# Kernel optimization log

Measured on AMD Instinct MI355X. Metric: run time of the kernel, lower is better.

The kernel has to match this reference:

```python
import jax, jax.numpy as jnp
import numpy as np

N, E = 50000, 500000
A, R, EB, EH, H, C, AH, SH, S, AV = 64, 20, 32, 64, 4, 32, 128, 64, 32, 32
EPS = 1e-8
MAX_DIST = 0.5   # nm, maximum_interaction_radius
SCALE = 1.0      # nm, scale_factor


def physnet_rbf(d):
    # PhysNet radial basis: exp(-beta * (exp(-d) - mu_k)^2), mu_k in [exp(-r_cut), 1]
    mu = jnp.linspace(np.exp(-MAX_DIST), 1.0, R).astype(jnp.float32)
    beta = jnp.float32((2.0 / R * (1.0 - np.exp(-MAX_DIST))) ** -2)
    return jnp.exp(-beta * (jnp.exp(-d)[:, None] - mu) ** 2)  # [E, R]


def _forward(h, x, v, idx_i, idx_j, W_edge_in, b_edge_in, W_edge_h, b_edge_h,
             W_edge_out, b_edge_out, W_att, b_att, W_x_mix, W_node1, b_node1,
             W_node2, b_node2, W_post1, b_post1, W_post2, b_post2,
             W_vel1, b_vel1, W_vel2, w_v_mix):
    n = h.shape[0]
    act = jax.nn.silu
    seg_sum = lambda t, idx: jax.ops.segment_sum(t, idx, num_segments=n)

    # geometry
    r_ij = x[idx_j] - x[idx_i]                       # [E,3]
    d_ij = jnp.sqrt(jnp.sum(r_ij * r_ij, -1) + EPS)  # [E]
    dir_ij = r_ij / (d_ij[:, None] + EPS)            # [E,3]

    # update_edge: gather, RBF filter, edge MLP
    h_cat = jnp.concatenate([h[idx_i], h[idx_j]], -1)                 # [E,2A]
    filtered = physnet_rbf(d_ij) * (h_cat @ W_edge_in + b_edge_in)    # [E,R]
    e_in = jnp.concatenate([h_cat, filtered, d_ij[:, None] / SCALE], -1)
    h_ij_edge = act(e_in @ W_edge_h + b_edge_h) @ W_edge_out + b_edge_out  # [E,EB]

    # semantic attention: CELU logits + segment softmax over receivers per head
    logits = jax.nn.celu(h_ij_edge @ W_att + b_att, alpha=2.0)        # [E,H]
    seg_max = jax.ops.segment_max(logits, idx_i, num_segments=n)      # [n,H]
    exp_l = jnp.exp(logits - seg_max[idx_i])
    denom = seg_sum(exp_l, idx_i)
    att = exp_l / (denom[idx_i] + EPS)                                # [E,H]
    h_ij_semantic = (att[:, :, None] * h_ij_edge[:, None, :]).reshape(-1, H * EB)

    # neighborhood aggregation (scatter-add)
    h_i_semantic = seg_sum(h_ij_semantic, idx_i)                      # [n,H*EB]

    # spatial attention
    mix = jnp.tanh(h_ij_semantic @ W_x_mix)                           # [E,C]
    combinations = dir_ij[:, None, :] * mix[:, :, None]               # [E,C,3]
    counts = jnp.maximum(seg_sum(jnp.ones((idx_i.shape[0],), h.dtype), idx_i), 1.0)
    comb_mean = seg_sum(combinations, idx_i) / counts[:, None, None]  # scatter-mean
    comb_norm2 = jnp.sum(comb_mean * comb_mean, -1)                   # [n,C]
    h_i_spatial = act(act(comb_norm2 @ W_post1 + b_post1) @ W_post2 + b_post2)

    # node update (residual)
    node_in = jnp.concatenate([h, h_i_semantic, h_i_spatial], -1)
    h_upd = h + act(act(node_in @ W_node1 + b_node1) @ W_node2 + b_node2)

    # velocity / coordinate update
    v_ij = jnp.einsum('ecx,c->ex', combinations, w_v_mix)             # [E,3]
    dv = seg_sum(v_ij, idx_i) / counts[:, None]                       # scatter-mean
    gate = 2.0 * jax.nn.sigmoid(act(h_upd @ W_vel1 + b_vel1) @ W_vel2)  # [n,1]
    v_upd = gate * v + dv
    x_upd = x + v_upd
    return h_upd, x_upd, v_upd


def _p(k, shape, scale=0.05):
    return jax.random.normal(k, shape, dtype=jnp.float32) * scale


def setup_inputs() -> dict:
    key = jax.random.key(0)
    ks = jax.random.split(key, 24)
    return {
        'h': jax.random.normal(ks[0], (N, A), dtype=jnp.float32),
        'x': jax.random.normal(ks[1], (N, 3), dtype=jnp.float32),
        'v': jax.random.normal(ks[2], (N, 3), dtype=jnp.float32),
        'idx_i': jax.random.randint(ks[3], (E,), 0, N),
        'idx_j': jax.random.randint(ks[4], (E,), 0, N),
        'W_edge_in': _p(ks[5], (2 * A, R)), 'b_edge_in': jnp.zeros((R,), jnp.float32),
        'W_edge_h': _p(ks[6], (2 * A + R + 1, EH)), 'b_edge_h': jnp.zeros((EH,), jnp.float32),
        'W_edge_out': _p(ks[7], (EH, EB)), 'b_edge_out': jnp.zeros((EB,), jnp.float32),
        'W_att': _p(ks[8], (EB, H)), 'b_att': jnp.zeros((H,), jnp.float32),
        'W_x_mix': _p(ks[9], (H * EB, C)),
        'W_node1': _p(ks[10], (A + H * EB + S, AH)), 'b_node1': jnp.zeros((AH,), jnp.float32),
        'W_node2': _p(ks[11], (AH, A)), 'b_node2': jnp.zeros((A,), jnp.float32),
        'W_post1': _p(ks[12], (C, SH)), 'b_post1': jnp.zeros((SH,), jnp.float32),
        'W_post2': _p(ks[13], (SH, S)), 'b_post2': jnp.zeros((S,), jnp.float32),
        'W_vel1': _p(ks[14], (A, AV)), 'b_vel1': jnp.zeros((AV,), jnp.float32),
        'W_vel2': _p(ks[15], (AV, 1)),
        'w_v_mix': _p(ks[16], (C,)),
    }


def reference(h, x, v, idx_i, idx_j, W_edge_in, b_edge_in, W_edge_h, b_edge_h,
              W_edge_out, b_edge_out, W_att, b_att, W_x_mix, W_node1, b_node1,
              W_node2, b_node2, W_post1, b_post1, W_post2, b_post2,
              W_vel1, b_vel1, W_vel2, w_v_mix):
    return _forward(h, x, v, idx_i, idx_j, W_edge_in, b_edge_in, W_edge_h, b_edge_h,
                    W_edge_out, b_edge_out, W_att, b_att, W_x_mix, W_node1, b_node1,
                    W_node2, b_node2, W_post1, b_post1, W_post2, b_post2,
                    W_vel1, b_vel1, W_vel2, w_v_mix)
```

## Files before the change

### kernel.cpp

```cpp
#include <hip/hip_runtime.h>
#include <math.h>

#define DA 64
#define NODEIN_DIM 224
#define EPSC 1e-8f

typedef short v8s __attribute__((ext_vector_type(8)));
typedef float v4f __attribute__((ext_vector_type(4)));
typedef unsigned short ushort_t;

__device__ __forceinline__ float siluf(float v) {
  return v * __builtin_amdgcn_rcpf(1.0f + __expf(-v));
}
__device__ __forceinline__ float tanhfast(float x) {
  return 1.0f - 2.0f * __builtin_amdgcn_rcpf(__expf(2.0f * x) + 1.0f);
}

__device__ __forceinline__ void atomAddF(float* p, float v) {
#if defined(__HIP_DEVICE_COMPILE__)
  unsafeAtomicAdd(p, v);
#else
  atomicAdd(p, v);
#endif
}

__device__ __forceinline__ unsigned short f2bfu(float f) {
  union { float f; unsigned u; } v; v.f = f;
  unsigned r = v.u + 0x7fffu + ((v.u >> 16) & 1u);
  return (unsigned short)(r >> 16);
}
__device__ __forceinline__ short f2bfs(float f) { return (short)f2bfu(f); }
__device__ __forceinline__ float bf2f(ushort_t s) {
  union { unsigned u; float f; } v; v.u = ((unsigned)s) << 16; return v.f;
}

#define MU0 0.60653065971263342f
#define DMU ((1.0f - 0.60653065971263342f) / 19.0f)
#define BETA ((float)(1.0 / (0.039346934028736658 * 0.039346934028736658)))

__global__ __launch_bounds__(256) void cast_count(
    const float* __restrict__ hsrc, ushort_t* __restrict__ hb, int n4,
    const int* __restrict__ idx_i, int* __restrict__ deg, int E)
{
  const int stride = gridDim.x * blockDim.x;
  for (int i = blockIdx.x * blockDim.x + threadIdx.x; i < n4; i += stride) {
    const float4 fv = ((const float4*)hsrc)[i];
    ushort4 o;
    o.x = f2bfu(fv.x); o.y = f2bfu(fv.y); o.z = f2bfu(fv.z); o.w = f2bfu(fv.w);
    ((ushort4*)hb)[i] = o;
  }
  for (int e = blockIdx.x * blockDim.x + threadIdx.x; e < E; e += stride)
    atomicAdd(&deg[idx_i[e]], 1);
}

#define SCAN_B 64
#define SCAN_T (SCAN_B * 256)

__global__ __launch_bounds__(256) void deg_tsum(
    const int* __restrict__ deg, int* __restrict__ tsum, int N, int C)
{
  const int g = blockIdx.x * blockDim.x + threadIdx.x;
  const int lo = g * C;
  const int hi = (lo + C < N) ? (lo + C) : N;
  int s = 0;
  for (int i = lo; i < hi; ++i) s += deg[i];
  tsum[g] = s;
}

__global__ __launch_bounds__(256) void scan_tsum(int* __restrict__ tsum)
{
  __shared__ int ps[256];
  const int t = threadIdx.x;
  const int per = SCAN_T / 256;
  const int lo = t * per;
  int s = 0;
  for (int i = 0; i < per; ++i) s += tsum[lo + i];
  ps[t] = s;
  __syncthreads();
  if (t == 0) {
    int a = 0;
    for (int i = 0; i < 256; ++i) { const int v = ps[i]; ps[i] = a; a += v; }
  }
  __syncthreads();
  int acc = ps[t];
  for (int i = 0; i < per; ++i) {
    const int v = tsum[lo + i];
    tsum[lo + i] = acc;
    acc += v;
  }
}

__global__ __launch_bounds__(256) void write_csr(
    const int* __restrict__ deg, const int* __restrict__ tpre,
    int* __restrict__ rowstart, int* __restrict__ cursor, int N, int C)
{
  const int g = blockIdx.x * blockDim.x + threadIdx.x;
  const int lo = g * C;
  const int hi = (lo + C < N) ? (lo + C) : N;
  int acc = tpre[g];
  for (int i = lo; i < hi; ++i) {
    const int d = deg[i];
    rowstart[i] = acc;
    cursor[i] = acc;
    acc += d;
  }
  if (hi == N) rowstart[N] = acc;
}

__global__ __launch_bounds__(256) void bucket_edges(
    const int* __restrict__ idx_i, const int* __restrict__ idx_j,
    int* __restrict__ cursor, int* __restrict__ iperm,
    int* __restrict__ jperm, int E)
{
  const int stride = gridDim.x * blockDim.x;
  for (int e = blockIdx.x * blockDim.x + threadIdx.x; e < E; e += stride) {
    const int ii = idx_i[e];
    const int pos = atomicAdd(&cursor[ii], 1);
    iperm[pos] = ii;
    jperm[pos] = idx_j[e];
  }
}

#define THS 72
__global__ __launch_bounds__(512, 6) void edge_f12(
    const ushort_t* __restrict__ h_bf, const float* __restrict__ x,
    const int* __restrict__ iperm, const int* __restrict__ jperm,
    const float* __restrict__ W_in, const float* __restrict__ b_in,
    const float* __restrict__ W_h, const float* __restrict__ b_h,
    const float* __restrict__ W_out, const float* __restrict__ b_out,
    const float* __restrict__ W_att, const float* __restrict__ b_att,
    float* __restrict__ dirb, ushort_t* __restrict__ heb,
    float* __restrict__ expl, float* __restrict__ denom, int E)
{
  __shared__ ushort_t sB1[8 * 512];
  __shared__ ushort_t sB2[20 * 512];
  __shared__ ushort_t tH[8][16 * THS];

  const int tid = threadIdx.x;
  const int bsz = blockDim.x;
  for (int idx = tid; idx < 8 * 512; idx += bsz) {
    const int j = idx & 7;
    const int ln = (idx >> 3) & 63;
    const int f = idx >> 9;
    const int k = (f >> 1) * 32 + (ln >> 4) * 8 + j;
    const int col = (f & 1) * 16 + (ln & 15);
    sB1[idx] = (col < 20) ? f2bfu(W_in[k * 20 + col]) : (ushort_t)0;
  }
  for (int idx = tid; idx < 20 * 512; idx += bsz) {
    const int j = idx & 7;
    const int ln = (idx >> 3) & 63;
    const int f = idx >> 9;
    const int k = (f >> 2) * 32 + (ln >> 4) * 8 + j;
    const int col = (f & 3) * 16 + (ln & 15);
    sB2[idx] = (k < 149) ? f2bfu(W_h[k * 64 + col]) : (ushort_t)0;
  }
  __syncthreads();

  const int gtid = blockIdx.x * blockDim.x + tid;
  const int wid = gtid >> 6;
  const int lane = tid & 63;
  const int w = tid >> 6;
  const int nw = (gridDim.x * blockDim.x) >> 6;
  const int l15 = lane & 15;
  const int q = lane >> 4;

  const ushort_t* b1l = sB1 + lane * 8;
  const ushort_t* b2l = sB2 + lane * 8;

  v8s bfr3[2][2];
  #pragma unroll
  for (int kc = 0; kc < 2; ++kc)
    #pragma unroll
    for (int nt = 0; nt < 2; ++nt)
      #pragma unroll
      for (int j = 0; j < 8; ++j) {
        const int k = kc * 32 + q * 8 + j;
        const int col = nt * 16 + l15;
        bfr3[kc][nt][j] = f2bfs(W_out[k * 32 + col]);
      }

  float bin[2], mu[2];
  #pragma unroll
  for (int nt = 0; nt < 2; ++nt) {
    const int col = nt * 16 + l15;
    bin[nt] = (col < 20) ? b_in[col] : 0.0f;
    mu[nt] = MU0 + (float)col * DMU;
  }
  float bias2[4];
  #pragma unroll
  for (int nt = 0; nt < 4; ++nt) bias2[nt] = b_h[nt * 16 + l15];
  float bias3[2];
  #pragma unroll
  for (int nt = 0; nt < 2; ++nt) bias3[nt] = b_out[nt * 16 + l15];

  v8s battf;
  #pragma unroll
  for (int j = 0; j < 8; ++j)
    battf[j] = (l15 < 4) ? f2bfs(W_att[(q * 8 + j) * 4 + l15]) : (short)0;
  const float bav = (l15 < 4) ? b_att[l15] : 0.0f;

  const int ntiles = (E + 15) >> 4;

  int iiC = 0, jjC = 0;
  v8s afr[4];
  float rCx = 0.f, rCy = 0.f, rCz = 0.f;
  if (wid < ntiles) {
    const int row0 = wid * 16 + l15;
    const int rowL0 = (row0 < E) ? row0 : (E - 1);
    iiC = iperm[rowL0];
    jjC = jperm[rowL0];
    afr[0] = *(const v8s*)(h_bf + (size_t)iiC * 64 + q * 8);
    afr[1] = *(const v8s*)(h_bf + (size_t)iiC * 64 + 32 + q * 8);
    afr[2] = *(const v8s*)(h_bf + (size_t)jjC * 64 + q * 8);
    afr[3] = *(const v8s*)(h_bf + (size_t)jjC * 64 + 32 + q * 8);
    if (lane < 16) {
      rCx = x[jjC * 3 + 0] - x[iiC * 3 + 0];
      rCy = x[jjC * 3 + 1] - x[iiC * 3 + 1];
      rCz = x[jjC * 3 + 2] - x[iiC * 3 + 2];
    }
  }

  for (int t = wid; t < ntiles; t += nw) {
    const int tn = t + nw;
    int iiN = 0, jjN = 0;
    v8s nfr[4];
    float rNx = 0.f, rNy = 0.f, rNz = 0.f;
    if (tn < ntiles) {
      const int rowN = tn * 16 + l15;
      const int rowLN = (rowN < E) ? rowN : (E - 1);
      iiN = iperm[rowLN];
      jjN = jperm[rowLN];
      nfr[0] = *(const v8s*)(h_bf + (size_t)iiN * 64 + q * 8);
      nfr[1] = *(const v8s*)(h_bf + (size_t)iiN * 64 + 32 + q * 8);
      nfr[2] = *(const v8s*)(h_bf + (size_t)jjN * 64 + q * 8);
      nfr[3] = *(const v8s*)(h_bf + (size_t)jjN * 64 + 32 + q * 8);
      if (lane < 16) {
        rNx = x[jjN * 3 + 0] - x[iiN * 3 + 0];
        rNy = x[jjN * 3 + 1] - x[iiN * 3 + 1];
        rNz = x[jjN * 3 + 2] - x[iiN * 3 + 2];
      }
    }

    const int row = t * 16 + l15;
    float dval = 0.0f;
    if (lane < 16) {
      const float s2 = rCx * rCx + rCy * rCy + rCz * rCz + EPSC;
      const float rv = __builtin_amdgcn_rsqf(s2);
      dval = s2 * rv;
      if (row < E) {
        dirb[row * 3 + 0] = rCx * rv;
        dirb[row * 3 + 1] = rCy * rv;
        dirb[row * 3 + 2] = rCz * rv;
      }
    }

    v4f acc1[2];
    #pragma unroll
    for (int nt = 0; nt < 2; ++nt) {
      v4f a = {0.f, 0.f, 0.f, 0.f};
      #pragma unroll
      for (int kc = 0; kc < 4; ++kc) {
        const v8s bfrag = *(const v8s*)(b1l + (kc * 2 + nt) * 512);
        a = __builtin_amdgcn_mfma_f32_16x16x32_bf16(afr[kc], bfrag, a, 0, 0, 0);
      }
      acc1[nt] = a;
    }

    float dr[4], edr[4];
    #pragma unroll
    for (int r = 0; r < 4; ++r) {
      dr[r] = __shfl(dval, q * 4 + r);
      edr[r] = __expf(-dr[r]);
    }
    #pragma unroll
    for (int nt = 0; nt < 2; ++nt) {
      const int col = nt * 16 + l15;
      #pragma unroll
      for (int r = 0; r < 4; ++r) {
        ushort_t ov;
        if (col < 20) {
          const float tt = edr[r] - mu[nt];
          ov = f2bfu((acc1[nt][r] + bin[nt]) * __expf(-BETA * tt * tt));
        } else if (col == 20) {
          ov = f2bfu(dr[r]);
        } else {
          ov = 0;
        }
        tH[w][(q * 4 + r) * THS + col] = ov;
      }
    }
    __builtin_amdgcn_wave_barrier();

    const v8s afr4 = *(const v8s*)&tH[w][l15 * THS + q * 8];
    __builtin_amdgcn_wave_barrier();

    v4f acc2[4];
    #pragma unroll
    for (int nt = 0; nt < 4; ++nt) {
      v4f a = {0.f, 0.f, 0.f, 0.f};
      #pragma unroll
      for (int kc = 0; kc < 4; ++kc) {
        const v8s bfrag = *(const v8s*)(b2l + (kc * 4 + nt) * 512);
        a = __builtin_amdgcn_mfma_f32_16x16x32_bf16(afr[kc], bfrag, a, 0, 0, 0);
      }
      const v8s bfrag4 = *(const v8s*)(b2l + (4 * 4 + nt) * 512);
      a = __builtin_amdgcn_mfma_f32_16x16x32_bf16(afr4, bfrag4, a, 0, 0, 0);
      acc2[nt] = a;
    }

    #pragma unroll
    for (int nt = 0; nt < 4; ++nt) {
      #pragma unroll
      for (int r = 0; r < 4; ++r)
        tH[w][(q * 4 + r) * THS + nt * 16 + l15] =
            f2bfu(siluf(acc2[nt][r] + bias2[nt]));
    }
    __builtin_amdgcn_wave_barrier();

    v8s af3[2];
    af3[0] = *(const v8s*)&tH[w][l15 * THS + q * 8];
    af3[1] = *(const v8s*)&tH[w][l15 * THS + 32 + q * 8];

    v4f acc3[2];
    #pragma unroll
    for (int nt = 0; nt < 2; ++nt) {
      v4f a = {0.f, 0.f, 0.f, 0.f};
      #pragma unroll
      for (int kc = 0; kc < 2; ++kc)
        a = __builtin_amdgcn_mfma_f32_16x16x32_bf16(af3[kc], bfr3[kc][nt], a, 0, 0, 0);
      acc3[nt] = a;
    }
    __builtin_amdgcn_wave_barrier();

    const int rowb = t * 16 + q * 4;
    #pragma unroll
    for (int nt = 0; nt < 2; ++nt) {
      const int col = nt * 16 + l15;
      #pragma unroll
      for (int r = 0; r < 4; ++r) {
        const ushort_t hv = f2bfu(acc3[nt][r] + bias3[nt]);
        tH[w][(q * 4 + r) * THS + col] = hv;
        if (rowb + r < E) heb[(size_t)(rowb + r) * 32 + col] = hv;
      }
    }
    __builtin_amdgcn_wave_barrier();

    const v8s afA = *(const v8s*)&tH[w][l15 * THS + q * 8];
    v4f az = {0.f, 0.f, 0.f, 0.f};
    const v4f aacc = __builtin_amdgcn_mfma_f32_16x16x32_bf16(afA, battf, az, 0, 0, 0);

    int ii_r[4];
    #pragma unroll
    for (int r = 0; r < 4; ++r) ii_r[r] = __shfl(iiC, q * 4 + r);

    if (l15 < 4) {
      #pragma unroll
      for (int r = 0; r < 4; ++r) {
        if (rowb + r < E) {
          const float la = aacc[r] + bav;
          const float l = (la > 0.f) ? la : 2.0f * (__expf(0.5f * la) - 1.0f);
          const float ev = __expf(l);
          expl[(size_t)(rowb + r) * 4 + l15] = ev;
          atomAddF(&denom[ii_r[r] * 4 + l15], ev);
        }
      }
    }
    __builtin_amdgcn_wave_barrier();

    iiC = iiN; jjC = jjN;
    afr[0] = nfr[0]; afr[1] = nfr[1]; afr[2] = nfr[2]; afr[3] = nfr[3];
    rCx = rNx; rCy = rNy; rCz = rNz;
  }
}

__global__ __launch_bounds__(256) void node_fused(
    const int* __restrict__ rowstart,
    const ushort_t* __restrict__ heb,
    const float* __restrict__ expl, const float* __restrict__ denom,
    const float* __restrict__ dirb,
    const float* __restrict__ W_xmix, const float* __restrict__ w_vmix,
    ushort_t* __restrict__ hsem, float* __restrict__ norm2,
    float* __restrict__ dv_mean, int N)
{
  __shared__ ushort_t sBX[8 * 512];

  const int tid = threadIdx.x;
  for (int idx = tid; idx < 8 * 512; idx += 256) {
    const int j = idx & 7;
    const int ln = (idx >> 3) & 63;
    const int f = idx >> 9;
    const int k = (f >> 1) * 32 + (ln >> 4) * 8 + j;
    const int col = (f & 1) * 16 + (ln & 15);
    sBX[idx] = f2bfu(W_xmix[k * 32 + col]);
  }
  __syncthreads();

  const int gtid = blockIdx.x * blockDim.x + tid;
  const int wid = gtid >> 6;
  const int lane = tid & 63;
  const int nw = (gridDim.x * blockDim.x) >> 6;
  const int l15 = lane & 15;
  const int q = lane >> 4;
  const int hh = lane >> 5;
  const int eb = lane & 31;
  const ushort_t* bXl = sBX + lane * 8;

  const float wv0 = w_vmix[l15];
  const float wv1 = w_vmix[16 + l15];

  for (int n = wid; n < N; n += nw) {
    const int s = rowstart[n];
    const int epd = rowstart[n + 1];
    const int deg = epd - s;

    float invden[4];
    #pragma unroll
    for (int h4 = 0; h4 < 4; ++h4)
      invden[h4] = __builtin_amdgcn_rcpf(denom[n * 4 + h4] + EPSC);

    float semA = 0.f, semB = 0.f;
    {
      int k = s;
      const int e4 = s + (deg & ~3);
      for (; k < e4; k += 4) {
        #pragma unroll
        for (int u = 0; u < 4; ++u) {
          const float he = bf2f(heb[(size_t)(k + u) * 32 + eb]);
          semA += expl[(size_t)(k + u) * 4 + hh] * he;
          semB += expl[(size_t)(k + u) * 4 + 2 + hh] * he;
        }
      }
      for (; k < epd; ++k) {
        const float he = bf2f(heb[(size_t)k * 32 + eb]);
        semA += expl[(size_t)k * 4 + hh] * he;
        semB += expl[(size_t)k * 4 + 2 + hh] * he;
      }
    }
    hsem[(size_t)n * 128 + lane] = f2bfu(semA * invden[hh]);
    hsem[(size_t)n * 128 + 64 + lane] = f2bfu(semB * invden[2 + hh]);

    float cx0 = 0.f, cy0 = 0.f, cz0 = 0.f;
    float cx1 = 0.f, cy1 = 0.f, cz1 = 0.f;
    float dvx = 0.f, dvy = 0.f, dvz = 0.f;

    for (int c0 = 0; c0 < deg; c0 += 16) {
      const int ra = c0 + l15;
      const int eA = s + ((ra < deg) ? ra : (deg - 1));
      const v8s hech = *(const v8s*)(heb + (size_t)eA * 32 + q * 8);

      v4f y[4][2];
      #pragma unroll
      for (int h4 = 0; h4 < 4; ++h4) {
        #pragma unroll
        for (int nt = 0; nt < 2; ++nt) {
          v4f z = {0.f, 0.f, 0.f, 0.f};
          y[h4][nt] = __builtin_amdgcn_mfma_f32_16x16x32_bf16(
              hech, *(const v8s*)(bXl + (h4 * 2 + nt) * 512), z, 0, 0, 0);
        }
      }

      #pragma unroll
      for (int r = 0; r < 4; ++r) {
        const int rr = c0 + q * 4 + r;
        const int live = rr < deg;
        const int eR = s + (live ? rr : (deg - 1));
        const float lf = live ? 1.0f : 0.0f;
        const float4 ex4 = *(const float4*)(expl + (size_t)eR * 4);
        const float at0 = ex4.x * invden[0] * lf;
        const float at1 = ex4.y * invden[1] * lf;
        const float at2 = ex4.z * invden[2] * lf;
        const float at3 = ex4.w * invden[3] * lf;
        const float p0 = at0 * y[0][0][r] + at1 * y[1][0][r] +
                         at2 * y[2][0][r] + at3 * y[3][0][r];
        const float p1 = at0 * y[0][1][r] + at1 * y[1][1][r] +
                         at2 * y[2][1][r] + at3 * y[3][1][r];
        const float dx = dirb[eR * 3 + 0];
        const float dy = dirb[eR * 3 + 1];
        const float dz = dirb[eR * 3 + 2];
        const float m0 = tanhfast(p0);
        const float m1 = tanhfast(p1);
        cx0 += dx * m0; cy0 += dy * m0; cz0 += dz * m0;
        cx1 += dx * m1; cy1 += dy * m1; cz1 += dz * m1;
        float pr = m0 * wv0 + m1 * wv1;
        pr += __shfl_xor(pr, 1);
        pr += __shfl_xor(pr, 2);
        pr += __shfl_xor(pr, 4);
        pr += __shfl_xor(pr, 8);
        if (l15 == 0) { dvx += pr * dx; dvy += pr * dy; dvz += pr * dz; }
      }
    }

    cx0 += __shfl_xor(cx0, 16); cx0 += __shfl_xor(cx0, 32);
    cy0 += __shfl_xor(cy0, 16); cy0 += __shfl_xor(cy0, 32);
    cz0 += __shfl_xor(cz0, 16); cz0 += __shfl_xor(cz0, 32);
    cx1 += __shfl_xor(cx1, 16); cx1 += __shfl_xor(cx1, 32);
    cy1 += __shfl_xor(cy1, 16); cy1 += __shfl_xor(cy1, 32);
    cz1 += __shfl_xor(cz1, 16); cz1 += __shfl_xor(cz1, 32);
    dvx += __shfl_xor(dvx, 16); dvx += __shfl_xor(dvx, 32);
    dvy += __shfl_xor(dvy, 16); dvy += __shfl_xor(dvy, 32);
    dvz += __shfl_xor(dvz, 16); dvz += __shfl_xor(dvz, 32);

    const float cinv = __builtin_amdgcn_rcpf(fmaxf((float)deg, 1.0f));
    if (lane < 16) {
      const float mx0 = cx0 * cinv, my0 = cy0 * cinv, mz0 = cz0 * cinv;
      norm2[(size_t)n * 32 + l15] = mx0 * mx0 + my0 * my0 + mz0 * mz0;
      const float mx1 = cx1 * cinv, my1 = cy1 * cinv, mz1 = cz1 * cinv;
      norm2[(size_t)n * 32 + 16 + l15] = mx1 * mx1 + my1 * my1 + mz1 * mz1;
    }
    if (lane == 0) {
      dv_mean[n * 3 + 0] = dvx * cinv;
      dv_mean[n * 3 + 1] = dvy * cinv;
      dv_mean[n * 3 + 2] = dvz * cinv;
    }
  }
}

#define W1S 232
__global__ __launch_bounds__(256) void node_c1_mfma(
    const ushort_t* __restrict__ h_bf, const ushort_t* __restrict__ hsem,
    const float* __restrict__ norm2,
    const float* __restrict__ W_post1, const float* __restrict__ b_post1,
    const float* __restrict__ W_post2, const float* __restrict__ b_post2,
    const float* __restrict__ W_node1, const float* __restrict__ b_node1,
    ushort_t* __restrict__ nh_out, int N)
{
  __shared__ ushort_t sW1t[128 * W1S];
  __shared__ ushort_t tp[4][16 * THS];

  const int tid = threadIdx.x;
  for (int idx = tid; idx < 224 * 128; idx += 256) {
    const int k = idx >> 7;
    const int c = idx & 127;
    sW1t[c * W1S + k] = f2bfu(W_node1[idx]);
  }
  __syncthreads();

  const int lane = tid & 63;
  const int w = tid >> 6;
  const int l15 = lane & 15;
  const int q = lane >> 4;

  v8s bp1[4];
  #pragma unroll
  for (int nt = 0; nt < 4; ++nt)
    #pragma unroll
    for (int j = 0; j < 8; ++j)
      bp1[nt][j] = f2bfs(W_post1[(q * 8 + j) * 64 + nt * 16 + l15]);
  v8s bp2[2][2];
  #pragma unroll
  for (int kc = 0; kc < 2; ++kc)
    #pragma unroll
    for (int nt = 0; nt < 2; ++nt)
      #pragma unroll
      for (int j = 0; j < 8; ++j)
        bp2[kc][nt][j] = f2bfs(W_post2[(kc * 32 + q * 8 + j) * 32 + nt * 16 + l15]);
  float bb1[4];
  #pragma unroll
  for (int nt = 0; nt < 4; ++nt) bb1[nt] = b_post1[nt * 16 + l15];
  float bb2[2];
  #pragma unroll
  for (int nt = 0; nt < 2; ++nt) bb2[nt] = b_post2[nt * 16 + l15];
  float b1[8];
  #pragma unroll
  for (int nt = 0; nt < 8; ++nt) b1[nt] = b_node1[nt * 16 + l15];

  const int gw = blockIdx.x * 4 + w;
  const int nwv = gridDim.x * 4;
  const int ntiles = (N + 15) >> 4;

  for (int t = gw; t < ntiles; t += nwv) {
    const int row = t * 16 + l15;
    const int rowL = (row < N) ? row : (N - 1);

    const float4 nA = *(const float4*)(norm2 + (size_t)rowL * 32 + q * 8);
    const float4 nB = *(const float4*)(norm2 + (size_t)rowL * 32 + q * 8 + 4);
    v8s a1;
    a1[0] = f2bfs(nA.x); a1[1] = f2bfs(nA.y);
    a1[2] = f2bfs(nA.z); a1[3] = f2bfs(nA.w);
    a1[4] = f2bfs(nB.x); a1[5] = f2bfs(nB.y);
    a1[6] = f2bfs(nB.z); a1[7] = f2bfs(nB.w);

    v4f p1[4];
    #pragma unroll
    for (int nt = 0; nt < 4; ++nt) {
      v4f a = {0.f, 0.f, 0.f, 0.f};
      p1[nt] = __builtin_amdgcn_mfma_f32_16x16x32_bf16(a1, bp1[nt], a, 0, 0, 0);
    }
    #pragma unroll
    for (int nt = 0; nt < 4; ++nt)
      #pragma unroll
      for (int r = 0; r < 4; ++r)
        tp[w][(q * 4 + r) * THS + nt * 16 + l15] =
            f2bfu(siluf(p1[nt][r] + bb1[nt]));
    __builtin_amdgcn_wave_barrier();

    v8s a2[2];
    a2[0] = *(const v8s*)&tp[w][l15 * THS + q * 8];
    a2[1] = *(const v8s*)&tp[w][l15 * THS + 32 + q * 8];

    v4f p2[2];
    #pragma unroll
    for (int nt = 0; nt < 2; ++nt) {
      v4f a = {0.f, 0.f, 0.f, 0.f};
      #pragma unroll
      for (int kc = 0; kc < 2; ++kc)
        a = __builtin_amdgcn_mfma_f32_16x16x32_bf16(a2[kc], bp2[kc][nt], a, 0, 0, 0);
      p2[nt] = a;
    }
    __builtin_amdgcn_wave_barrier();
    #pragma unroll
    for (int nt = 0; nt < 2; ++nt)
      #pragma unroll
      for (int r = 0; r < 4; ++r)
        tp[w][(q * 4 + r) * THS + nt * 16 + l15] =
            f2bfu(siluf(p2[nt][r] + bb2[nt]));
    __builtin_amdgcn_wave_barrier();

    v8s af[7];
    af[0] = *(const v8s*)(h_bf + (size_t)rowL * 64 + q * 8);
    af[1] = *(const v8s*)(h_bf + (size_t)rowL * 64 + 32 + q * 8);
    #pragma unroll
    for (int kc = 0; kc < 4; ++kc)
      af[2 + kc] = *(const v8s*)(hsem + (size_t)rowL * 128 + kc * 32 + q * 8);
    af[6] = *(const v8s*)&tp[w][l15 * THS + q * 8];

    v4f acc[8];
    #pragma unroll
    for (int nt = 0; nt < 8; ++nt) acc[nt] = (v4f){0.f, 0.f, 0.f, 0.f};
    #pragma unroll
    for (int kc = 0; kc < 7; ++kc) {
      #pragma unroll
      for (int nt = 0; nt < 8; ++nt) {
        const v8s bfrag =
            *(const v8s*)&sW1t[(nt * 16 + l15) * W1S + kc * 32 + q * 8];
        acc[nt] = __builtin_amdgcn_mfma_f32_16x16x32_bf16(af[kc], bfrag, acc[nt], 0, 0, 0);
      }
    }

    const int rowb = t * 16 + q * 4;
    #pragma unroll
    for (int nt = 0; nt < 8; ++nt) {
      #pragma unroll
      for (int r = 0; r < 4; ++r)
        if (rowb + r < N)
          nh_out[(size_t)(rowb + r) * 128 + nt * 16 + l15] =
              f2bfu(siluf(acc[nt][r] + b1[nt]));
    }
  }
}

__global__ __launch_bounds__(256) void node_c2_mfma(
    const float* __restrict__ h, const float* __restrict__ x,
    const float* __restrict__ v, const ushort_t* __restrict__ nh,
    const float* __restrict__ dv_mean,
    const float* __restrict__ W_node2, const float* __restrict__ b_node2,
    const float* __restrict__ W_vel1, const float* __restrict__ b_vel1,
    const float* __restrict__ W_vel2,
    float* __restrict__ out, int N)
{
  __shared__ ushort_t sW2[16 * 64 * 8];
  __shared__ ushort_t sWv[4 * 64 * 8];
  __shared__ ushort_t tH[4][16 * THS];
  __shared__ float sg[4][16];

  const int tid = threadIdx.x;
  for (int idx = tid; idx < 16 * 64 * 8; idx += 256) {
    const int j = idx & 7;
    const int ln = (idx >> 3) & 63;
    const int f = idx >> 9;
    const int k = (f >> 2) * 32 + (ln >> 4) * 8 + j;
    const int col = (f & 3) * 16 + (ln & 15);
    sW2[idx] = f2bfu(W_node2[k * 64 + col]);
  }
  for (int idx = tid; idx < 4 * 64 * 8; idx += 256) {
    const int j = idx & 7;
    const int ln = (idx >> 3) & 63;
    const int f = idx >> 9;
    const int k = (f >> 1) * 32 + (ln >> 4) * 8 + j;
    const int col = (f & 1) * 16 + (ln & 15);
    sWv[idx] = f2bfu(W_vel1[k * 32 + col]);
  }
  __syncthreads();

  const int lane = tid & 63;
  const int w = tid >> 6;
  const int l15 = lane & 15;
  const int q = lane >> 4;

  const ushort_t* w2l = sW2 + lane * 8;
  const ushort_t* wvl = sWv + lane * 8;

  float b2[4];
  #pragma unroll
  for (int nt = 0; nt < 4; ++nt) b2[nt] = b_node2[nt * 16 + l15];
  float bv[2];
  #pragma unroll
  for (int nt = 0; nt < 2; ++nt) bv[nt] = b_vel1[nt * 16 + l15];
  float wv2[2];
  #pragma unroll
  for (int nt = 0; nt < 2; ++nt) wv2[nt] = W_vel2[nt * 16 + l15];

  const int gw = blockIdx.x * 4 + w;
  const int nwv = gridDim.x * 4;
  const int ntiles = (N + 15) >> 4;

  for (int t = gw; t < ntiles; t += nwv) {
    const int row = t * 16 + l15;
    const int rowL = (row < N) ? row : (N - 1);

    v8s af[4];
    #pragma unroll
    for (int kc = 0; kc < 4; ++kc)
      af[kc] = *(const v8s*)(nh + (size_t)rowL * 128 + kc * 32 + q * 8);

    v4f acc[4];
    #pragma unroll
    for (int nt = 0; nt < 4; ++nt) {
      v4f a = {0.f, 0.f, 0.f, 0.f};
      #pragma unroll
      for (int kc = 0; kc < 4; ++kc) {
        const v8s bfrag = *(const v8s*)(w2l + (kc * 4 + nt) * 512);
        a = __builtin_amdgcn_mfma_f32_16x16x32_bf16(af[kc], bfrag, a, 0, 0, 0);
      }
      acc[nt] = a;
    }

    const int rowb = t * 16 + q * 4;
    #pragma unroll
    for (int nt = 0; nt < 4; ++nt) {
      const int col = nt * 16 + l15;
      #pragma unroll
      for (int r = 0; r < 4; ++r) {
        const int n = rowb + r;
        if (n < N) {
          const float hu = h[(size_t)n * 64 + col] + siluf(acc[nt][r] + b2[nt]);
          out[(size_t)n * 64 + col] = hu;
          tH[w][(q * 4 + r) * THS + col] = f2bfu(hu);
        }
      }
    }
    __builtin_amdgcn_wave_barrier();

    v8s a2[2];
    a2[0] = *(const v8s*)&tH[w][l15 * THS + q * 8];
    a2[1] = *(const v8s*)&tH[w][l15 * THS + 32 + q * 8];
    v4f av[2];
    #pragma unroll
    for (int nt = 0; nt < 2; ++nt) {
      v4f a = {0.f, 0.f, 0.f, 0.f};
      #pragma unroll
      for (int kc = 0; kc < 2; ++kc) {
        const v8s bfrag = *(const v8s*)(wvl + (kc * 2 + nt) * 512);
        a = __builtin_amdgcn_mfma_f32_16x16x32_bf16(a2[kc], bfrag, a, 0, 0, 0);
      }
      av[nt] = a;
    }

    #pragma unroll
    for (int r = 0; r < 4; ++r) {
      float pr = siluf(av[0][r] + bv[0]) * wv2[0] +
                 siluf(av[1][r] + bv[1]) * wv2[1];
      pr += __shfl_xor(pr, 1);
      pr += __shfl_xor(pr, 2);
      pr += __shfl_xor(pr, 4);
      pr += __shfl_xor(pr, 8);
      if (l15 == 0)
        sg[w][q * 4 + r] = 2.0f * __builtin_amdgcn_rcpf(1.0f + __expf(-pr));
    }
    __builtin_amdgcn_wave_barrier();

    if (lane < 48) {
      const int rr = lane / 3;
      const int c = lane % 3;
      const int n = t * 16 + rr;
      if (n < N) {
        const float gate = sg[w][rr];
        const float dv = dv_mean[n * 3 + c];
        const float vu = gate * v[n * 3 + c] + dv;
        out[(size_t)N * 64 + (size_t)n * 3 + c] = x[n * 3 + c] + vu;
        out[(size_t)N * 64 + (size_t)N * 3 + (size_t)n * 3 + c] = vu;
      }
    }
    __builtin_amdgcn_wave_barrier();
  }
}

extern "C" void kernel_launch(void* const* d_in, const int* in_sizes, int n_in,
                              void* d_out, int out_size, void* d_ws, size_t ws_size,
                              hipStream_t stream) {
  const float* h   = (const float*)d_in[0];
  const float* x   = (const float*)d_in[1];
  const float* v   = (const float*)d_in[2];
  const int* idx_i = (const int*)d_in[3];
  const int* idx_j = (const int*)d_in[4];
  const float* W_edge_in  = (const float*)d_in[5];
  const float* b_edge_in  = (const float*)d_in[6];
  const float* W_edge_h   = (const float*)d_in[7];
  const float* b_edge_h   = (const float*)d_in[8];
  const float* W_edge_out = (const float*)d_in[9];
  const float* b_edge_out = (const float*)d_in[10];
  const float* W_att      = (const float*)d_in[11];
  const float* b_att      = (const float*)d_in[12];
  const float* W_x_mix    = (const float*)d_in[13];
  const float* W_node1    = (const float*)d_in[14];
  const float* b_node1    = (const float*)d_in[15];
  const float* W_node2    = (const float*)d_in[16];
  const float* b_node2    = (const float*)d_in[17];
  const float* W_post1    = (const float*)d_in[18];
  const float* b_post1    = (const float*)d_in[19];
  const float* W_post2    = (const float*)d_in[20];
  const float* b_post2    = (const float*)d_in[21];
  const float* W_vel1     = (const float*)d_in[22];
  const float* b_vel1     = (const float*)d_in[23];
  const float* W_vel2     = (const float*)d_in[24];
  const float* w_v_mix    = (const float*)d_in[25];

  const int E = in_sizes[3];
  const int N = in_sizes[0] / DA;

  float* ws = (float*)d_ws;
  size_t off = 0;
  float* denom    = ws + off; off += (size_t)N * 4;
  int*   deg      = (int*)(ws + off); off += (size_t)N;
  const size_t zeroBytes = off * sizeof(float);
  int*   rowstart = (int*)(ws + off); off += (size_t)N + 4;
  int*   cursor   = (int*)(ws + off); off += (size_t)N;
  int*   tsum     = (int*)(ws + off); off += (size_t)SCAN_T;
  int*   iperm    = (int*)(ws + off); off += (size_t)E;
  int*   jperm    = (int*)(ws + off); off += (size_t)E;
  float* expl     = ws + off; off += (size_t)E * 4;
  float* dirb     = ws + off; off += (size_t)E * 3;
  float* hsemR    = ws + off; off += (size_t)N * 64;
  float* norm2    = ws + off; off += (size_t)N * 32;
  float* dv_mean  = ws + off; off += (size_t)N * 4;
  float* hbfR     = ws + off; off += (size_t)N * 32;
  float* fltR     = ws + off; off += (size_t)E * 16;
  float* hebR     = ws + off; off += (size_t)E * 16;

  ushort_t* h_bf = (ushort_t*)hbfR;
  ushort_t* hsem = (ushort_t*)hsemR;
  ushort_t* heb  = (ushort_t*)hebR;
  ushort_t* nh   = (ushort_t*)fltR;

  hipMemsetAsync(d_ws, 0, zeroBytes, stream);

  {
    const int n4 = (N * 64) / 4;
    cast_count<<<1024, 256, 0, stream>>>(h, h_bf, n4, idx_i, deg, E);
  }
  {
    const int C = (N + SCAN_T - 1) / SCAN_T;
    deg_tsum<<<SCAN_B, 256, 0, stream>>>(deg, tsum, N, C);
    scan_tsum<<<1, 256, 0, stream>>>(tsum);
    write_csr<<<SCAN_B, 256, 0, stream>>>(deg, tsum, rowstart, cursor, N, C);
  }
  bucket_edges<<<512, 256, 0, stream>>>(idx_i, idx_j, cursor, iperm, jperm, E);
  edge_f12<<<768, 512, 0, stream>>>(h_bf, x, iperm, jperm,
                                    W_edge_in, b_edge_in, W_edge_h, b_edge_h,
                                    W_edge_out, b_edge_out, W_att, b_att,
                                    dirb, heb, expl, denom, E);
  node_fused<<<2048, 256, 0, stream>>>(rowstart, heb, expl, denom, dirb,
                                       W_x_mix, w_v_mix, hsem, norm2,
                                       dv_mean, N);
  node_c1_mfma<<<512, 256, 0, stream>>>(
      h_bf, hsem, norm2, W_post1, b_post1, W_post2, b_post2,
      W_node1, b_node1, nh, N);
  node_c2_mfma<<<512, 256, 0, stream>>>(
      h, x, v, nh, dv_mean, W_node2, b_node2, W_vel1, b_vel1, W_vel2,
      (float*)d_out, N);
}
```

Baseline: 393.3 us.

## Pack edge index pairs and direction vectors, shrink edge kernel blocks

Interleaves the bucketed receiver and sender indices into one int2 array so each edge needs a single 8-byte load. Pads the per-edge direction buffer to a float4 that also carries the distance, so each edge is written and read with one vector access. The edge kernel also moves from 512-thread blocks with an occupancy hint to 256-thread blocks with more of them, which halves per-block shared memory for the transpose tile. The cost is an extra float of storage per edge and a different occupancy and weight-staging balance.

```diff
diff --git a/kernel.cpp b/kernel.cpp
--- a/kernel.cpp
+++ b/kernel.cpp
@@ -109,36 +109,33 @@
 
 __global__ __launch_bounds__(256) void bucket_edges(
     const int* __restrict__ idx_i, const int* __restrict__ idx_j,
-    int* __restrict__ cursor, int* __restrict__ iperm,
-    int* __restrict__ jperm, int E)
+    int* __restrict__ cursor, int2* __restrict__ ijperm, int E)
 {
   const int stride = gridDim.x * blockDim.x;
   for (int e = blockIdx.x * blockDim.x + threadIdx.x; e < E; e += stride) {
     const int ii = idx_i[e];
     const int pos = atomicAdd(&cursor[ii], 1);
-    iperm[pos] = ii;
-    jperm[pos] = idx_j[e];
+    ijperm[pos] = make_int2(ii, idx_j[e]);
   }
 }
 
 #define THS 72
-__global__ __launch_bounds__(512, 6) void edge_f12(
+__global__ __launch_bounds__(256) void edge_f12(
     const ushort_t* __restrict__ h_bf, const float* __restrict__ x,
-    const int* __restrict__ iperm, const int* __restrict__ jperm,
+    const int2* __restrict__ ijperm,
     const float* __restrict__ W_in, const float* __restrict__ b_in,
     const float* __restrict__ W_h, const float* __restrict__ b_h,
     const float* __restrict__ W_out, const float* __restrict__ b_out,
     const float* __restrict__ W_att, const float* __restrict__ b_att,
-    float* __restrict__ dirb, ushort_t* __restrict__ heb,
+    float4* __restrict__ dirb, ushort_t* __restrict__ heb,
     float* __restrict__ expl, float* __restrict__ denom, int E)
 {
   __shared__ ushort_t sB1[8 * 512];
   __shared__ ushort_t sB2[20 * 512];
-  __shared__ ushort_t tH[8][16 * THS];
+  __shared__ ushort_t tH[4][16 * THS];
 
   const int tid = threadIdx.x;
-  const int bsz = blockDim.x;
-  for (int idx = tid; idx < 8 * 512; idx += bsz) {
+  for (int idx = tid; idx < 8 * 512; idx += 256) {
     const int j = idx & 7;
     const int ln = (idx >> 3) & 63;
     const int f = idx >> 9;
@@ -146,7 +143,7 @@
     const int col = (f & 1) * 16 + (ln & 15);
     sB1[idx] = (col < 20) ? f2bfu(W_in[k * 20 + col]) : (ushort_t)0;
   }
-  for (int idx = tid; idx < 20 * 512; idx += bsz) {
+  for (int idx = tid; idx < 20 * 512; idx += 256) {
     const int j = idx & 7;
     const int ln = (idx >> 3) & 63;
     const int f = idx >> 9;
@@ -207,8 +204,9 @@
   if (wid < ntiles) {
     const int row0 = wid * 16 + l15;
     const int rowL0 = (row0 < E) ? row0 : (E - 1);
-    iiC = iperm[rowL0];
-    jjC = jperm[rowL0];
+    const int2 ij = ijperm[rowL0];
+    iiC = ij.x;
+    jjC = ij.y;
     afr[0] = *(const v8s*)(h_bf + (size_t)iiC * 64 + q * 8);
     afr[1] = *(const v8s*)(h_bf + (size_t)iiC * 64 + 32 + q * 8);
     afr[2] = *(const v8s*)(h_bf + (size_t)jjC * 64 + q * 8);
@@ -228,8 +226,9 @@
     if (tn < ntiles) {
       const int rowN = tn * 16 + l15;
       const int rowLN = (rowN < E) ? rowN : (E - 1);
-      iiN = iperm[rowLN];
-      jjN = jperm[rowLN];
+      const int2 ij = ijperm[rowLN];
+      iiN = ij.x;
+      jjN = ij.y;
       nfr[0] = *(const v8s*)(h_bf + (size_t)iiN * 64 + q * 8);
       nfr[1] = *(const v8s*)(h_bf + (size_t)iiN * 64 + 32 + q * 8);
       nfr[2] = *(const v8s*)(h_bf + (size_t)jjN * 64 + q * 8);
@@ -248,9 +247,9 @@
       const float rv = __builtin_amdgcn_rsqf(s2);
       dval = s2 * rv;
       if (row < E) {
-        dirb[row * 3 + 0] = rCx * rv;
-        dirb[row * 3 + 1] = rCy * rv;
-        dirb[row * 3 + 2] = rCz * rv;
+        float4 dq;
+        dq.x = rCx * rv; dq.y = rCy * rv; dq.z = rCz * rv; dq.w = dval;
+        dirb[row] = dq;
       }
     }
 
@@ -377,7 +376,7 @@
     const int* __restrict__ rowstart,
     const ushort_t* __restrict__ heb,
     const float* __restrict__ expl, const float* __restrict__ denom,
-    const float* __restrict__ dirb,
+    const float4* __restrict__ dirb,
     const float* __restrict__ W_xmix, const float* __restrict__ w_vmix,
     ushort_t* __restrict__ hsem, float* __restrict__ norm2,
     float* __restrict__ dv_mean, int N)
@@ -474,19 +473,17 @@
                          at2 * y[2][0][r] + at3 * y[3][0][r];
         const float p1 = at0 * y[0][1][r] + at1 * y[1][1][r] +
                          at2 * y[2][1][r] + at3 * y[3][1][r];
-        const float dx = dirb[eR * 3 + 0];
-        const float dy = dirb[eR * 3 + 1];
-        const float dz = dirb[eR * 3 + 2];
+        const float4 dq = dirb[eR];
         const float m0 = tanhfast(p0);
         const float m1 = tanhfast(p1);
-        cx0 += dx * m0; cy0 += dy * m0; cz0 += dz * m0;
-        cx1 += dx * m1; cy1 += dy * m1; cz1 += dz * m1;
+        cx0 += dq.x * m0; cy0 += dq.y * m0; cz0 += dq.z * m0;
+        cx1 += dq.x * m1; cy1 += dq.y * m1; cz1 += dq.z * m1;
         float pr = m0 * wv0 + m1 * wv1;
         pr += __shfl_xor(pr, 1);
         pr += __shfl_xor(pr, 2);
         pr += __shfl_xor(pr, 4);
         pr += __shfl_xor(pr, 8);
-        if (l15 == 0) { dvx += pr * dx; dvy += pr * dy; dvz += pr * dz; }
+        if (l15 == 0) { dvx += pr * dq.x; dvy += pr * dq.y; dvz += pr * dq.z; }
       }
     }
 
@@ -826,10 +823,9 @@
   int*   rowstart = (int*)(ws + off); off += (size_t)N + 4;
   int*   cursor   = (int*)(ws + off); off += (size_t)N;
   int*   tsum     = (int*)(ws + off); off += (size_t)SCAN_T;
-  int*   iperm    = (int*)(ws + off); off += (size_t)E;
-  int*   jperm    = (int*)(ws + off); off += (size_t)E;
+  int2*  ijperm   = (int2*)(ws + off); off += (size_t)E * 2;
   float* expl     = ws + off; off += (size_t)E * 4;
-  float* dirb     = ws + off; off += (size_t)E * 3;
+  float* dirbR    = ws + off; off += (size_t)E * 4;
   float* hsemR    = ws + off; off += (size_t)N * 64;
   float* norm2    = ws + off; off += (size_t)N * 32;
   float* dv_mean  = ws + off; off += (size_t)N * 4;
@@ -841,6 +837,7 @@
   ushort_t* hsem = (ushort_t*)hsemR;
   ushort_t* heb  = (ushort_t*)hebR;
   ushort_t* nh   = (ushort_t*)fltR;
+  float4*   dirb = (float4*)dirbR;
 
   hipMemsetAsync(d_ws, 0, zeroBytes, stream);
 
@@ -854,11 +851,11 @@
     scan_tsum<<<1, 256, 0, stream>>>(tsum);
     write_csr<<<SCAN_B, 256, 0, stream>>>(deg, tsum, rowstart, cursor, N, C);
   }
-  bucket_edges<<<512, 256, 0, stream>>>(idx_i, idx_j, cursor, iperm, jperm, E);
-  edge_f12<<<768, 512, 0, stream>>>(h_bf, x, iperm, jperm,
-                                    W_edge_in, b_edge_in, W_edge_h, b_edge_h,
-                                    W_edge_out, b_edge_out, W_att, b_att,
-                                    dirb, heb, expl, denom, E);
+  bucket_edges<<<512, 256, 0, stream>>>(idx_i, idx_j, cursor, ijperm, E);
+  edge_f12<<<1024, 256, 0, stream>>>(h_bf, x, ijperm,
+                                     W_edge_in, b_edge_in, W_edge_h, b_edge_h,
+                                     W_edge_out, b_edge_out, W_att, b_att,
+                                     dirb, heb, expl, denom, E);
   node_fused<<<2048, 256, 0, stream>>>(rowstart, heb, expl, denom, dirb,
                                        W_x_mix, w_v_mix, hsem, norm2,
                                        dv_mean, N);
```

New measurement: 350.9 us. -10.8%, faster.
